# Performance work log

Measured on AMD Instinct MI355X. Metric: run time of the kernel, lower is better.

Reference implementation:

```python
import jax, jax.numpy as jnp
import numpy as np

N = 10000      # nodes
E = 320000     # edges (avg degree 32)
D_IN = 128
D_H = 256
D_C = 32       # comm_dim
D_OUT = 64


def setup_inputs() -> dict:
    key = jax.random.key(0)
    ks = jax.random.split(key, 14)
    p = lambda k, shape: jax.random.normal(k, shape, jnp.float32) * 0.02
    return {
        "x": jax.random.normal(ks[0], (N, D_IN), jnp.float32),
        "edge_index": jax.random.randint(ks[1], (2, E), 0, N),
        "W_in": p(ks[2], (D_IN, D_H)), "b_in": jnp.zeros((D_H,), jnp.float32),
        "Wq": p(ks[3], (D_H, D_C)),   "bq": jnp.zeros((D_C,), jnp.float32),
        "Wk": p(ks[4], (D_H, D_C)),   "bk": jnp.zeros((D_C,), jnp.float32),
        "Wv": p(ks[5], (D_H, D_H)),   "bv": jnp.zeros((D_H,), jnp.float32),
        "W1": p(ks[6], (2 * D_H, D_H)), "b1": jnp.zeros((D_H,), jnp.float32),
        "W2": p(ks[7], (D_H, D_OUT)),  "b2": jnp.zeros((D_OUT,), jnp.float32),
    }


def reference(x, edge_index, W_in, b_in, Wq, bq, Wk, bk, Wv, bv, W1, b1, W2, b2):
    n = x.shape[0]
    h = x @ W_in + b_in                       # [N, D_H]
    q = h @ Wq + bq                           # [N, D_C]
    k = h @ Wk + bk                           # [N, D_C]
    v = h @ Wv + bv                           # [N, D_H]
    scores = (q @ k.T) / np.sqrt(q.shape[-1]).astype(np.float32)  # [N, N]
    # torch: zeros -> scatter 1 at edges -> masked_fill(==0, -inf);
    # edge positions keep value 1.0 ADDED to scores (faithful quirk).
    mask = jnp.full((n, n), -jnp.inf, jnp.float32)
    mask = mask.at[edge_index[0], edge_index[1]].set(1.0)
    w = jax.nn.softmax(scores + mask, axis=-1)
    w = jnp.nan_to_num(w, nan=0.0)            # rows with no edges -> all zeros
    comm = w @ v                              # [N, D_H]
    combined = jnp.concatenate([h, comm], axis=-1)  # [N, 2*D_H]
    return jax.nn.relu(combined @ W1 + b1) @ W2 + b2  # [N, D_OUT]
```

## Files before the change

### kernel.cpp

```cpp
#include <hip/hip_runtime.h>
#include <stdint.h>
#include <stddef.h>

constexpr int N_NODES = 10000;
constexpr int N_EDGES = 320000;
constexpr int DIM_IN  = 128;
constexpr int DIM_H   = 256;
constexpr int DIM_C   = 32;
constexpr int DIM_OUT = 64;
constexpr int DIM_QKV = DIM_C + DIM_C + DIM_H;
constexpr int DIM_QK  = 2 * DIM_C;
constexpr int DIM_CAT = 2 * DIM_H;
constexpr float SCALE = 0.17677669529663687f;
constexpr int MAXD = 192;
constexpr float VSCALE = 64.0f;

#if __has_builtin(__builtin_amdgcn_cvt_pk_f32_fp8) && __has_builtin(__builtin_amdgcn_cvt_pk_fp8_f32)
#define V_FP8 1
#else
#define V_FP8 0
#endif

constexpr size_t alignw(size_t w) { return (w + 15) & ~size_t(15); }
constexpr size_t OFF_DEG    = 0;
constexpr size_t OFF_COL    = alignw(OFF_DEG + N_NODES);
constexpr size_t OFF_QK     = alignw(OFF_COL + (size_t)N_NODES * MAXD);
constexpr size_t OFF_BQKV   = alignw(OFF_QK + (size_t)N_NODES * DIM_QK);
constexpr size_t OFF_VBF    = alignw(OFF_BQKV + DIM_QKV);
constexpr size_t OFF_XBF    = alignw(OFF_VBF + (size_t)N_NODES * DIM_H / 2);
constexpr size_t OFF_CATBF  = alignw(OFF_XBF + (size_t)N_NODES * DIM_IN / 2);
constexpr size_t OFF_WINT   = alignw(OFF_CATBF + (size_t)N_NODES * DIM_CAT / 2);
constexpr size_t OFF_WQKVT  = alignw(OFF_WINT + (size_t)DIM_H * DIM_IN / 2);
constexpr size_t OFF_W1T    = alignw(OFF_WQKVT + (size_t)DIM_QKV * DIM_H / 2);
constexpr size_t OFF_W2T    = alignw(OFF_W1T + (size_t)DIM_H * DIM_CAT / 2);

typedef __attribute__((ext_vector_type(8))) short short8;
typedef __attribute__((ext_vector_type(4))) float floatx4;
typedef __attribute__((ext_vector_type(2))) float floatx2;

__device__ inline unsigned short f2bf(float f) {
    uint32_t u = __builtin_bit_cast(uint32_t, f);
    uint32_t r = (u + 0x7fffu + ((u >> 16) & 1u)) >> 16;
    return (unsigned short)r;
}
__device__ inline float bf2f_lo(uint32_t u) { return __builtin_bit_cast(float, u << 16); }
__device__ inline float bf2f_hi(uint32_t u) { return __builtin_bit_cast(float, u & 0xffff0000u); }

template <bool RELU, int MODE>
__global__ __launch_bounds__(256)
void mfma_gemm(const unsigned short* __restrict__ A, int lda,
               const unsigned short* __restrict__ Bt,
               const float* __restrict__ bias,
               float* __restrict__ Cf, unsigned short* __restrict__ Cb, int ldc,
               int M, int K)
{
    constexpr int BM = 128, BN = 64, PAD = 40;
    __shared__ short As[BM * PAD];
    __shared__ short Bs[BN * PAD];
    const int tid   = threadIdx.x;
    const int wave  = tid >> 6;
    const int lane  = tid & 63;
    const int quad  = lane >> 4;
    const int col16 = lane & 15;
    const int row0  = blockIdx.y * BM;
    const int col0  = blockIdx.x * BN;

    floatx4 acc[2][4] = {};

    const int sr = tid >> 2;
    const int sc = (tid & 3) * 8;

    for (int k0 = 0; k0 < K; k0 += 32) {
        #pragma unroll
        for (int i = 0; i < 2; ++i) {
            int r = sr + i * 64;
            int gr = row0 + r;
            short8 v = {};
            if (gr < M) v = *(const short8*)(A + (size_t)gr * lda + k0 + sc);
            *(short8*)(As + r * PAD + sc) = v;
        }
        {
            short8 v = *(const short8*)(Bt + (size_t)(col0 + sr) * K + k0 + sc);
            *(short8*)(Bs + sr * PAD + sc) = v;
        }
        __syncthreads();
        short8 a0 = *(const short8*)(As + (wave * 32 + col16) * PAD + quad * 8);
        short8 a1 = *(const short8*)(As + (wave * 32 + 16 + col16) * PAD + quad * 8);
        #pragma unroll
        for (int nf = 0; nf < 4; ++nf) {
            short8 b = *(const short8*)(Bs + (nf * 16 + col16) * PAD + quad * 8);
            acc[0][nf] = __builtin_amdgcn_mfma_f32_16x16x32_bf16(a0, b, acc[0][nf], 0, 0, 0);
            acc[1][nf] = __builtin_amdgcn_mfma_f32_16x16x32_bf16(a1, b, acc[1][nf], 0, 0, 0);
        }
        __syncthreads();
    }
    #pragma unroll
    for (int mf = 0; mf < 2; ++mf)
        #pragma unroll
        for (int r = 0; r < 4; ++r) {
            int gr = row0 + wave * 32 + mf * 16 + quad * 4 + r;
            if (gr >= M) continue;
            #pragma unroll
            for (int nf = 0; nf < 4; ++nf) {
                int gc = col0 + nf * 16 + col16;
                float v = acc[mf][nf][r] + bias[gc];
                if (RELU) v = fmaxf(v, 0.f);
                if (MODE == 2) {
                    if (gc < DIM_QK) {
                        Cf[(size_t)gr * DIM_QK + gc] = v;
                    } else {
#if V_FP8
                        int pk = __builtin_amdgcn_cvt_pk_fp8_f32(v * VSCALE, 0.f, 0, false);
                        ((unsigned char*)Cb)[(size_t)gr * DIM_H + (gc - DIM_QK)] =
                            (unsigned char)(pk & 0xff);
#else
                        Cb[(size_t)gr * DIM_H + (gc - DIM_QK)] = f2bf(v);
#endif
                    }
                } else {
                    Cb[(size_t)gr * ldc + gc] = f2bf(v);
                }
            }
        }
}

__global__ __launch_bounds__(256)
void gemm_w1w2(const unsigned short* __restrict__ cat, const unsigned short* __restrict__ W1T,
               const float* __restrict__ b1, const unsigned short* __restrict__ W2T,
               const float* __restrict__ b2, float* __restrict__ out, int M)
{
    constexpr int PAD = 40, TP = 260;
    __shared__ short As[64 * PAD];
    __shared__ short BsTs[64 * TP];
    short* Bs = BsTs;
    short* Ts = BsTs;
    const int tid   = threadIdx.x;
    const int wave  = tid >> 6;
    const int lane  = tid & 63;
    const int quad  = lane >> 4;
    const int col16 = lane & 15;
    const int row0  = blockIdx.x * 64;

    const int sr = tid >> 2;
    const int sc = (tid & 3) * 8;

    floatx4 acc[16] = {};
    for (int k0 = 0; k0 < DIM_CAT; k0 += 32) {
        {
            int gr = row0 + sr;
            short8 v = {};
            if (gr < M) v = *(const short8*)(cat + (size_t)gr * DIM_CAT + k0 + sc);
            *(short8*)(As + sr * PAD + sc) = v;
        }
        #pragma unroll
        for (int p = 0; p < 4; ++p) {
            int r = sr + p * 64;
            *(short8*)(Bs + r * PAD + sc) = *(const short8*)(W1T + (size_t)r * DIM_CAT + k0 + sc);
        }
        __syncthreads();
        short8 a = *(const short8*)(As + (wave * 16 + col16) * PAD + quad * 8);
        #pragma unroll
        for (int nf = 0; nf < 16; ++nf) {
            short8 b = *(const short8*)(Bs + (nf * 16 + col16) * PAD + quad * 8);
            acc[nf] = __builtin_amdgcn_mfma_f32_16x16x32_bf16(a, b, acc[nf], 0, 0, 0);
        }
        __syncthreads();
    }

    #pragma unroll
    for (int nf = 0; nf < 16; ++nf) {
        int gc = nf * 16 + col16;
        float bia = b1[gc];
        #pragma unroll
        for (int r = 0; r < 4; ++r) {
            int lr = wave * 16 + quad * 4 + r;
            float v = fmaxf(acc[nf][r] + bia, 0.f);
            Ts[lr * TP + gc] = (short)f2bf(v);
        }
    }
    __syncthreads();

    floatx4 acc2[4] = {};
    for (int k0 = 0; k0 < DIM_H; k0 += 32) {
        short8 a = *(const short8*)(Ts + (wave * 16 + col16) * TP + k0 + quad * 8);
        #pragma unroll
        for (int nf = 0; nf < 4; ++nf) {
            int brow = nf * 16 + col16;
            short8 b = *(const short8*)(W2T + (size_t)brow * DIM_H + k0 + quad * 8);
            acc2[nf] = __builtin_amdgcn_mfma_f32_16x16x32_bf16(a, b, acc2[nf], 0, 0, 0);
        }
    }
    #pragma unroll
    for (int nf = 0; nf < 4; ++nf) {
        int gc = nf * 16 + col16;
        float bia = b2[gc];
        #pragma unroll
        for (int r = 0; r < 4; ++r) {
            int gr = row0 + wave * 16 + quad * 4 + r;
            if (gr < M) out[(size_t)gr * DIM_OUT + gc] = acc2[nf][r] + bia;
        }
    }
}

__global__ void zero_deg(int* __restrict__ deg) {
    int i = blockIdx.x * blockDim.x + threadIdx.x;
    if (i < N_NODES) deg[i] = 0;
}

__global__ void prep_all(const float* __restrict__ x, const int* __restrict__ ei,
                         const float* __restrict__ W_in,
                         const float* __restrict__ Wq, const float* __restrict__ Wk,
                         const float* __restrict__ Wv,
                         const float* __restrict__ bq, const float* __restrict__ bk,
                         const float* __restrict__ bv,
                         const float* __restrict__ W1, const float* __restrict__ W2,
                         int* __restrict__ deg, int* __restrict__ col,
                         unsigned short* __restrict__ xb,
                         unsigned short* __restrict__ WinT, unsigned short* __restrict__ WqkvT,
                         unsigned short* __restrict__ W1T, unsigned short* __restrict__ W2T,
                         float* __restrict__ bqkv)
{
    int i = blockIdx.x * blockDim.x + threadIdx.x;
    int stride = gridDim.x * blockDim.x;
    for (int e = i; e < N_EDGES; e += stride) {
        int src = ei[e];
        int dst = ei[N_EDGES + e];
        int slot = atomicAdd(&deg[src], 1);
        if (slot < MAXD) col[src * MAXD + slot] = dst;
    }
    for (int idx = i; idx < (N_NODES * DIM_IN) / 8; idx += stride) {
        float4 a = ((const float4*)x)[2 * idx];
        float4 b = ((const float4*)x)[2 * idx + 1];
        uint4 o;
        o.x = (uint32_t)f2bf(a.x) | ((uint32_t)f2bf(a.y) << 16);
        o.y = (uint32_t)f2bf(a.z) | ((uint32_t)f2bf(a.w) << 16);
        o.z = (uint32_t)f2bf(b.x) | ((uint32_t)f2bf(b.y) << 16);
        o.w = (uint32_t)f2bf(b.z) | ((uint32_t)f2bf(b.w) << 16);
        ((uint4*)xb)[idx] = o;
    }
    for (int idx = i; idx < DIM_H * DIM_IN; idx += stride) {
        int n = idx / DIM_IN, k = idx % DIM_IN;
        WinT[idx] = f2bf(W_in[k * DIM_H + n]);
    }
    for (int idx = i; idx < DIM_QKV * DIM_H; idx += stride) {
        int n = idx / DIM_H, k = idx % DIM_H;
        float v = (n < DIM_C)     ? Wq[k * DIM_C + n]
                : (n < 2 * DIM_C) ? Wk[k * DIM_C + (n - DIM_C)]
                                  : Wv[k * DIM_H + (n - 2 * DIM_C)];
        WqkvT[idx] = f2bf(v);
    }
    for (int idx = i; idx < DIM_H * DIM_CAT; idx += stride) {
        int n = idx / DIM_CAT, k = idx % DIM_CAT;
        W1T[idx] = f2bf(W1[k * DIM_H + n]);
    }
    for (int idx = i; idx < DIM_OUT * DIM_H; idx += stride) {
        int n = idx / DIM_H, k = idx % DIM_H;
        W2T[idx] = f2bf(W2[k * DIM_OUT + n]);
    }
    for (int idx = i; idx < DIM_QKV; idx += stride)
        bqkv[idx] = (idx < DIM_C) ? bq[idx]
                  : (idx < 2 * DIM_C) ? bk[idx - DIM_C] : bv[idx - 2 * DIM_C];
}

__global__ __launch_bounds__(256)
void attn_row(const float* __restrict__ qk, const unsigned short* __restrict__ v_tab,
              const int* __restrict__ deg, const int* __restrict__ col,
              unsigned short* __restrict__ cat_bf) {
    __shared__ int   dstS[4][MAXD];
    __shared__ float wS[4][MAXD];
    __shared__ float qS[4][DIM_C];
    const int wave = threadIdx.x >> 6;
    const int lane = threadIdx.x & 63;
    const int row = blockIdx.x * 4 + wave;
    int d = deg[row];
    if (d > MAXD) d = MAXD;
    const int* crow = col + (size_t)row * MAXD;

    for (int p = lane; p < d; p += 64) dstS[wave][p] = crow[p];
    if (lane < DIM_C) qS[wave][lane] = qk[(size_t)row * DIM_QK + lane];
    __syncthreads();

    float mysum = 0.f;
    if (d <= 64) {
        int mydst = (lane < d) ? dstS[wave][lane] : -1;
        bool dup = false;
        #pragma unroll
        for (int k = 0; k < 63; ++k) {
            int other = __shfl(mydst, k, 64);
            dup = dup || (k < lane && other == mydst);
        }
        float w = 0.f;
        if (lane < d && !dup) {
            const float4* kp = (const float4*)(qk + (size_t)mydst * DIM_QK + DIM_C);
            float s = 0.f;
            #pragma unroll
            for (int i = 0; i < DIM_C / 4; ++i) {
                float4 b = kp[i];
                s += qS[wave][4 * i + 0] * b.x + qS[wave][4 * i + 1] * b.y
                   + qS[wave][4 * i + 2] * b.z + qS[wave][4 * i + 3] * b.w;
            }
            w = expf(s * SCALE);
        }
        wS[wave][lane] = w;
        mysum = w;
    } else {
        for (int p = lane; p < d; p += 64) {
            int mydst = dstS[wave][p];
            bool dup = false;
            for (int j = 0; j < p; ++j) dup = dup || (dstS[wave][j] == mydst);
            float w = 0.f;
            if (!dup) {
                const float4* kp = (const float4*)(qk + (size_t)mydst * DIM_QK + DIM_C);
                float s = 0.f;
                #pragma unroll
                for (int i = 0; i < DIM_C / 4; ++i) {
                    float4 b = kp[i];
                    s += qS[wave][4 * i + 0] * b.x + qS[wave][4 * i + 1] * b.y
                       + qS[wave][4 * i + 2] * b.z + qS[wave][4 * i + 3] * b.w;
                }
                w = expf(s * SCALE);
            }
            wS[wave][p] = w;
            mysum += w;
        }
    }
    #pragma unroll
    for (int off = 32; off; off >>= 1) mysum += __shfl_down(mysum, off, 64);
    float total = __shfl(mysum, 0, 64);
#if V_FP8
    float inv = (d > 0 && total > 0.f) ? 1.0f / (total * VSCALE) : 0.f;
#else
    float inv = (d > 0 && total > 0.f) ? 1.0f / total : 0.f;
#endif
    __syncthreads();

    float4 acc = make_float4(0.f, 0.f, 0.f, 0.f);
#if V_FP8
    const uint32_t* vb = (const uint32_t*)v_tab;
#else
    const uint2* vb = (const uint2*)v_tab;
#endif
    for (int p0 = 0; p0 < d; p0 += 16) {
        int j[16]; float w[16];
        #pragma unroll
        for (int t = 0; t < 16; ++t) {
            int idx = p0 + t;
            bool in = idx < d;
            j[t] = in ? dstS[wave][idx] : 0;
            w[t] = in ? wS[wave][idx] : 0.f;
        }
#if V_FP8
        uint32_t r[16];
        #pragma unroll
        for (int t = 0; t < 16; ++t) r[t] = vb[(size_t)j[t] * 64 + lane];
        #pragma unroll
        for (int t = 0; t < 16; ++t) {
            floatx2 lo = __builtin_amdgcn_cvt_pk_f32_fp8(r[t], false);
            floatx2 hi = __builtin_amdgcn_cvt_pk_f32_fp8(r[t], true);
            acc.x += w[t] * lo.x; acc.y += w[t] * lo.y;
            acc.z += w[t] * hi.x; acc.w += w[t] * hi.y;
        }
#else
        uint2 r[16];
        #pragma unroll
        for (int t = 0; t < 16; ++t) r[t] = vb[(size_t)j[t] * 64 + lane];
        #pragma unroll
        for (int t = 0; t < 16; ++t) {
            acc.x += w[t] * bf2f_lo(r[t].x);
            acc.y += w[t] * bf2f_hi(r[t].x);
            acc.z += w[t] * bf2f_lo(r[t].y);
            acc.w += w[t] * bf2f_hi(r[t].y);
        }
#endif
    }
    acc.x *= inv; acc.y *= inv; acc.z *= inv; acc.w *= inv;
    uint2 o;
    o.x = (uint32_t)f2bf(acc.x) | ((uint32_t)f2bf(acc.y) << 16);
    o.y = (uint32_t)f2bf(acc.z) | ((uint32_t)f2bf(acc.w) << 16);
    *(uint2*)(cat_bf + (size_t)row * DIM_CAT + DIM_H + lane * 4) = o;
}

extern "C" void kernel_launch(void* const* d_in, const int* in_sizes, int n_in,
                              void* d_out, int out_size, void* d_ws, size_t ws_size,
                              hipStream_t stream) {
    (void)in_sizes; (void)n_in; (void)out_size; (void)ws_size;
    const float* x    = (const float*)d_in[0];
    const int*   ei   = (const int*)d_in[1];
    const float* W_in = (const float*)d_in[2];
    const float* b_in = (const float*)d_in[3];
    const float* Wq   = (const float*)d_in[4];
    const float* bq   = (const float*)d_in[5];
    const float* Wk   = (const float*)d_in[6];
    const float* bk   = (const float*)d_in[7];
    const float* Wv   = (const float*)d_in[8];
    const float* bv   = (const float*)d_in[9];
    const float* W1   = (const float*)d_in[10];
    const float* b1   = (const float*)d_in[11];
    const float* W2   = (const float*)d_in[12];
    const float* b2   = (const float*)d_in[13];
    float* out = (float*)d_out;

    uint32_t* ws      = (uint32_t*)d_ws;
    int*      deg     = (int*)(ws + OFF_DEG);
    int*      col     = (int*)(ws + OFF_COL);
    float*    qk      = (float*)(ws + OFF_QK);
    float*    bqkv    = (float*)(ws + OFF_BQKV);
    unsigned short* v_tab  = (unsigned short*)(ws + OFF_VBF);
    unsigned short* x_bf   = (unsigned short*)(ws + OFF_XBF);
    unsigned short* cat_bf = (unsigned short*)(ws + OFF_CATBF);
    unsigned short* WinT   = (unsigned short*)(ws + OFF_WINT);
    unsigned short* WqkvT  = (unsigned short*)(ws + OFF_WQKVT);
    unsigned short* W1T    = (unsigned short*)(ws + OFF_W1T);
    unsigned short* W2T    = (unsigned short*)(ws + OFF_W2T);

    zero_deg<<<(N_NODES + 255) / 256, 256, 0, stream>>>(deg);
    prep_all<<<640, 256, 0, stream>>>(x, ei, W_in, Wq, Wk, Wv, bq, bk, bv, W1, W2,
                                      deg, col, x_bf, WinT, WqkvT, W1T, W2T, bqkv);

    const int MB = (N_NODES + 127) / 128;
    mfma_gemm<false, 1><<<dim3(DIM_H / 64, MB), 256, 0, stream>>>(
        x_bf, DIM_IN, WinT, b_in, nullptr, cat_bf, DIM_CAT, N_NODES, DIM_IN);
    mfma_gemm<false, 2><<<dim3(DIM_QKV / 64, MB), 256, 0, stream>>>(
        cat_bf, DIM_CAT, WqkvT, bqkv, qk, v_tab, 0, N_NODES, DIM_H);
    attn_row<<<N_NODES / 4, 256, 0, stream>>>(qk, v_tab, deg, col, cat_bf);
    gemm_w1w2<<<(N_NODES + 63) / 64, 256, 0, stream>>>(
        cat_bf, W1T, b1, W2T, b2, out, N_NODES);
}
```

Baseline: 177.9 us.

## Fuse input projection and QKV GEMMs, convert x to bf16 on the fly

Merges the x@W_in GEMM and the QKV GEMM into one kernel that keeps the h tile in shared memory, so h is not reloaded from global memory for the second GEMM. The fp32 to bf16 conversion of x moves into that GEMM's load path, which drops the separate x_bf buffer and its pass in the prep kernel. The weight-transpose loops in prep now read coalesced and write strided. The zero_deg kernel becomes a memset, and the duplicate-check loop in attention is bounded by degree. The fused kernel uses a large shared-memory footprint and one block per 64 rows, which may reduce occupancy.

```diff
diff --git a/kernel.cpp b/kernel.cpp
--- a/kernel.cpp
+++ b/kernel.cpp
@@ -14,6 +14,8 @@
 constexpr float SCALE = 0.17677669529663687f;
 constexpr int MAXD = 192;
 constexpr float VSCALE = 64.0f;
+constexpr int PAD = 40;
+constexpr int HP  = 264;
 
 #if __has_builtin(__builtin_amdgcn_cvt_pk_f32_fp8) && __has_builtin(__builtin_amdgcn_cvt_pk_fp8_f32)
 #define V_FP8 1
@@ -22,21 +24,22 @@
 #endif
 
 constexpr size_t alignw(size_t w) { return (w + 15) & ~size_t(15); }
-constexpr size_t OFF_DEG    = 0;
-constexpr size_t OFF_COL    = alignw(OFF_DEG + N_NODES);
-constexpr size_t OFF_QK     = alignw(OFF_COL + (size_t)N_NODES * MAXD);
-constexpr size_t OFF_BQKV   = alignw(OFF_QK + (size_t)N_NODES * DIM_QK);
-constexpr size_t OFF_VBF    = alignw(OFF_BQKV + DIM_QKV);
-constexpr size_t OFF_XBF    = alignw(OFF_VBF + (size_t)N_NODES * DIM_H / 2);
-constexpr size_t OFF_CATBF  = alignw(OFF_XBF + (size_t)N_NODES * DIM_IN / 2);
-constexpr size_t OFF_WINT   = alignw(OFF_CATBF + (size_t)N_NODES * DIM_CAT / 2);
-constexpr size_t OFF_WQKVT  = alignw(OFF_WINT + (size_t)DIM_H * DIM_IN / 2);
-constexpr size_t OFF_W1T    = alignw(OFF_WQKVT + (size_t)DIM_QKV * DIM_H / 2);
-constexpr size_t OFF_W2T    = alignw(OFF_W1T + (size_t)DIM_H * DIM_CAT / 2);
+constexpr size_t OFF_DEG   = 0;
+constexpr size_t OFF_COL   = alignw(OFF_DEG + N_NODES);
+constexpr size_t OFF_QK    = alignw(OFF_COL + (size_t)N_NODES * MAXD);
+constexpr size_t OFF_BQKV  = alignw(OFF_QK + (size_t)N_NODES * DIM_QK);
+constexpr size_t OFF_VT    = alignw(OFF_BQKV + DIM_QKV);
+constexpr size_t OFF_CATBF = alignw(OFF_VT + (size_t)N_NODES * DIM_H / 2);
+constexpr size_t OFF_WINT  = alignw(OFF_CATBF + (size_t)N_NODES * DIM_CAT / 2);
+constexpr size_t OFF_WQKVT = alignw(OFF_WINT + (size_t)DIM_H * DIM_IN / 2);
+constexpr size_t OFF_W1T   = alignw(OFF_WQKVT + (size_t)DIM_QKV * DIM_H / 2);
+constexpr size_t OFF_W2T   = alignw(OFF_W1T + (size_t)DIM_H * DIM_CAT / 2);
 
 typedef __attribute__((ext_vector_type(8))) short short8;
 typedef __attribute__((ext_vector_type(4))) float floatx4;
 typedef __attribute__((ext_vector_type(2))) float floatx2;
+
+#define MFMA16 __builtin_amdgcn_mfma_f32_16x16x32_bf16
 
 __device__ inline unsigned short f2bf(float f) {
     uint32_t u = __builtin_bit_cast(uint32_t, f);
@@ -46,220 +49,156 @@
 __device__ inline float bf2f_lo(uint32_t u) { return __builtin_bit_cast(float, u << 16); }
 __device__ inline float bf2f_hi(uint32_t u) { return __builtin_bit_cast(float, u & 0xffff0000u); }
 
-template <bool RELU, int MODE>
+__global__ void prep(const int* __restrict__ ei,
+                     const float* __restrict__ W_in,
+                     const float* __restrict__ Wq, const float* __restrict__ Wk,
+                     const float* __restrict__ Wv,
+                     const float* __restrict__ bq, const float* __restrict__ bk,
+                     const float* __restrict__ bv,
+                     const float* __restrict__ W1, const float* __restrict__ W2,
+                     int* __restrict__ deg, int* __restrict__ col,
+                     unsigned short* __restrict__ WinT, unsigned short* __restrict__ WqkvT,
+                     unsigned short* __restrict__ W1T, unsigned short* __restrict__ W2T,
+                     float* __restrict__ bqkv)
+{
+    const int i0 = blockIdx.x * blockDim.x + threadIdx.x;
+    const int stride = gridDim.x * blockDim.x;
+    for (int e = i0; e < N_EDGES; e += stride) {
+        int src = ei[e];
+        int dst = ei[N_EDGES + e];
+        int slot = atomicAdd(&deg[src], 1);
+        if (slot < MAXD) col[src * MAXD + slot] = dst;
+    }
+    for (int idx = i0; idx < DIM_IN * DIM_H; idx += stride) {
+        int k = idx >> 8, n = idx & 255;
+        WinT[n * DIM_IN + k] = f2bf(W_in[idx]);
+    }
+    for (int idx = i0; idx < DIM_H * DIM_C; idx += stride) {
+        int k = idx >> 5, n = idx & 31;
+        WqkvT[n * DIM_H + k] = f2bf(Wq[idx]);
+    }
+    for (int idx = i0; idx < DIM_H * DIM_C; idx += stride) {
+        int k = idx >> 5, n = idx & 31;
+        WqkvT[(DIM_C + n) * DIM_H + k] = f2bf(Wk[idx]);
+    }
+    for (int idx = i0; idx < DIM_H * DIM_H; idx += stride) {
+        int k = idx >> 8, n = idx & 255;
+        WqkvT[(2 * DIM_C + n) * DIM_H + k] = f2bf(Wv[idx]);
+    }
+    for (int idx = i0; idx < DIM_CAT * DIM_H; idx += stride) {
+        int k = idx >> 8, n = idx & 255;
+        W1T[n * DIM_CAT + k] = f2bf(W1[idx]);
+    }
+    for (int idx = i0; idx < DIM_H * DIM_OUT; idx += stride) {
+        int k = idx >> 6, n = idx & 63;
+        W2T[n * DIM_H + k] = f2bf(W2[idx]);
+    }
+    for (int idx = i0; idx < DIM_QKV; idx += stride)
+        bqkv[idx] = (idx < DIM_C) ? bq[idx]
+                  : (idx < 2 * DIM_C) ? bk[idx - DIM_C] : bv[idx - 2 * DIM_C];
+}
+
 __global__ __launch_bounds__(256)
-void mfma_gemm(const unsigned short* __restrict__ A, int lda,
-               const unsigned short* __restrict__ Bt,
-               const float* __restrict__ bias,
-               float* __restrict__ Cf, unsigned short* __restrict__ Cb, int ldc,
-               int M, int K)
+void gemm12(const float* __restrict__ x,
+            const unsigned short* __restrict__ WinT, const float* __restrict__ b_in,
+            const unsigned short* __restrict__ WqkvT, const float* __restrict__ bqkv,
+            unsigned short* __restrict__ cat_bf, float* __restrict__ qk,
+            unsigned short* __restrict__ v_tab)
 {
-    constexpr int BM = 128, BN = 64, PAD = 40;
-    __shared__ short As[BM * PAD];
-    __shared__ short Bs[BN * PAD];
+    __shared__ short hS[64 * HP];
+    __shared__ short Bs[320 * PAD];
+    short* As = Bs + 256 * PAD;
     const int tid   = threadIdx.x;
     const int wave  = tid >> 6;
     const int lane  = tid & 63;
     const int quad  = lane >> 4;
     const int col16 = lane & 15;
-    const int row0  = blockIdx.y * BM;
-    const int col0  = blockIdx.x * BN;
-
-    floatx4 acc[2][4] = {};
-
-    const int sr = tid >> 2;
-    const int sc = (tid & 3) * 8;
-
-    for (int k0 = 0; k0 < K; k0 += 32) {
-        #pragma unroll
-        for (int i = 0; i < 2; ++i) {
-            int r = sr + i * 64;
-            int gr = row0 + r;
-            short8 v = {};
-            if (gr < M) v = *(const short8*)(A + (size_t)gr * lda + k0 + sc);
-            *(short8*)(As + r * PAD + sc) = v;
-        }
-        {
-            short8 v = *(const short8*)(Bt + (size_t)(col0 + sr) * K + k0 + sc);
-            *(short8*)(Bs + sr * PAD + sc) = v;
-        }
-        __syncthreads();
-        short8 a0 = *(const short8*)(As + (wave * 32 + col16) * PAD + quad * 8);
-        short8 a1 = *(const short8*)(As + (wave * 32 + 16 + col16) * PAD + quad * 8);
-        #pragma unroll
-        for (int nf = 0; nf < 4; ++nf) {
-            short8 b = *(const short8*)(Bs + (nf * 16 + col16) * PAD + quad * 8);
-            acc[0][nf] = __builtin_amdgcn_mfma_f32_16x16x32_bf16(a0, b, acc[0][nf], 0, 0, 0);
-            acc[1][nf] = __builtin_amdgcn_mfma_f32_16x16x32_bf16(a1, b, acc[1][nf], 0, 0, 0);
-        }
-        __syncthreads();
-    }
-    #pragma unroll
-    for (int mf = 0; mf < 2; ++mf)
-        #pragma unroll
-        for (int r = 0; r < 4; ++r) {
-            int gr = row0 + wave * 32 + mf * 16 + quad * 4 + r;
-            if (gr >= M) continue;
-            #pragma unroll
-            for (int nf = 0; nf < 4; ++nf) {
-                int gc = col0 + nf * 16 + col16;
-                float v = acc[mf][nf][r] + bias[gc];
-                if (RELU) v = fmaxf(v, 0.f);
-                if (MODE == 2) {
-                    if (gc < DIM_QK) {
-                        Cf[(size_t)gr * DIM_QK + gc] = v;
-                    } else {
-#if V_FP8
-                        int pk = __builtin_amdgcn_cvt_pk_fp8_f32(v * VSCALE, 0.f, 0, false);
-                        ((unsigned char*)Cb)[(size_t)gr * DIM_H + (gc - DIM_QK)] =
-                            (unsigned char)(pk & 0xff);
-#else
-                        Cb[(size_t)gr * DIM_H + (gc - DIM_QK)] = f2bf(v);
-#endif
-                    }
-                } else {
-                    Cb[(size_t)gr * ldc + gc] = f2bf(v);
-                }
-            }
-        }
-}
-
-__global__ __launch_bounds__(256)
-void gemm_w1w2(const unsigned short* __restrict__ cat, const unsigned short* __restrict__ W1T,
-               const float* __restrict__ b1, const unsigned short* __restrict__ W2T,
-               const float* __restrict__ b2, float* __restrict__ out, int M)
-{
-    constexpr int PAD = 40, TP = 260;
-    __shared__ short As[64 * PAD];
-    __shared__ short BsTs[64 * TP];
-    short* Bs = BsTs;
-    short* Ts = BsTs;
-    const int tid   = threadIdx.x;
-    const int wave  = tid >> 6;
-    const int lane  = tid & 63;
-    const int quad  = lane >> 4;
-    const int col16 = lane & 15;
+    const int sr    = tid >> 2;
+    const int sc    = (tid & 3) * 8;
     const int row0  = blockIdx.x * 64;
 
-    const int sr = tid >> 2;
-    const int sc = (tid & 3) * 8;
-
     floatx4 acc[16] = {};
-    for (int k0 = 0; k0 < DIM_CAT; k0 += 32) {
+    for (int k0 = 0; k0 < DIM_IN; k0 += 32) {
         {
             int gr = row0 + sr;
-            short8 v = {};
-            if (gr < M) v = *(const short8*)(cat + (size_t)gr * DIM_CAT + k0 + sc);
-            *(short8*)(As + sr * PAD + sc) = v;
+            float4 a = {}, b = {};
+            if (gr < N_NODES) {
+                const float4* xp = (const float4*)(x + (size_t)gr * DIM_IN + k0 + sc);
+                a = xp[0]; b = xp[1];
+            }
+            uint4 o;
+            o.x = (uint32_t)f2bf(a.x) | ((uint32_t)f2bf(a.y) << 16);
+            o.y = (uint32_t)f2bf(a.z) | ((uint32_t)f2bf(a.w) << 16);
+            o.z = (uint32_t)f2bf(b.x) | ((uint32_t)f2bf(b.y) << 16);
+            o.w = (uint32_t)f2bf(b.z) | ((uint32_t)f2bf(b.w) << 16);
+            *(uint4*)(As + sr * PAD + sc) = o;
         }
         #pragma unroll
         for (int p = 0; p < 4; ++p) {
             int r = sr + p * 64;
-            *(short8*)(Bs + r * PAD + sc) = *(const short8*)(W1T + (size_t)r * DIM_CAT + k0 + sc);
-        }
-        __syncthreads();
-        short8 a = *(const short8*)(As + (wave * 16 + col16) * PAD + quad * 8);
+            *(short8*)(Bs + r * PAD + sc) = *(const short8*)(WinT + (size_t)r * DIM_IN + k0 + sc);
+        }
+        __syncthreads();
+        short8 af = *(const short8*)(As + (wave * 16 + col16) * PAD + quad * 8);
         #pragma unroll
         for (int nf = 0; nf < 16; ++nf) {
-            short8 b = *(const short8*)(Bs + (nf * 16 + col16) * PAD + quad * 8);
-            acc[nf] = __builtin_amdgcn_mfma_f32_16x16x32_bf16(a, b, acc[nf], 0, 0, 0);
-        }
-        __syncthreads();
-    }
-
+            short8 bf = *(const short8*)(Bs + (nf * 16 + col16) * PAD + quad * 8);
+            acc[nf] = MFMA16(af, bf, acc[nf], 0, 0, 0);
+        }
+        __syncthreads();
+    }
     #pragma unroll
     for (int nf = 0; nf < 16; ++nf) {
         int gc = nf * 16 + col16;
-        float bia = b1[gc];
+        float bia = b_in[gc];
         #pragma unroll
         for (int r = 0; r < 4; ++r) {
             int lr = wave * 16 + quad * 4 + r;
-            float v = fmaxf(acc[nf][r] + bia, 0.f);
-            Ts[lr * TP + gc] = (short)f2bf(v);
+            unsigned short hv = f2bf(acc[nf][r] + bia);
+            hS[lr * HP + gc] = (short)hv;
+            if (row0 + lr < N_NODES) cat_bf[(size_t)(row0 + lr) * DIM_CAT + gc] = hv;
         }
     }
     __syncthreads();
 
-    floatx4 acc2[4] = {};
+    floatx4 acc2[20] = {};
     for (int k0 = 0; k0 < DIM_H; k0 += 32) {
-        short8 a = *(const short8*)(Ts + (wave * 16 + col16) * TP + k0 + quad * 8);
-        #pragma unroll
-        for (int nf = 0; nf < 4; ++nf) {
-            int brow = nf * 16 + col16;
-            short8 b = *(const short8*)(W2T + (size_t)brow * DIM_H + k0 + quad * 8);
-            acc2[nf] = __builtin_amdgcn_mfma_f32_16x16x32_bf16(a, b, acc2[nf], 0, 0, 0);
-        }
+        #pragma unroll
+        for (int p = 0; p < 5; ++p) {
+            int r = sr + p * 64;
+            *(short8*)(Bs + r * PAD + sc) = *(const short8*)(WqkvT + (size_t)r * DIM_H + k0 + sc);
+        }
+        __syncthreads();
+        short8 af = *(const short8*)(hS + (wave * 16 + col16) * HP + k0 + quad * 8);
+        #pragma unroll
+        for (int nf = 0; nf < 20; ++nf) {
+            short8 bf = *(const short8*)(Bs + (nf * 16 + col16) * PAD + quad * 8);
+            acc2[nf] = MFMA16(af, bf, acc2[nf], 0, 0, 0);
+        }
+        __syncthreads();
     }
     #pragma unroll
-    for (int nf = 0; nf < 4; ++nf) {
+    for (int nf = 0; nf < 20; ++nf) {
         int gc = nf * 16 + col16;
-        float bia = b2[gc];
+        float bia = bqkv[gc];
         #pragma unroll
         for (int r = 0; r < 4; ++r) {
             int gr = row0 + wave * 16 + quad * 4 + r;
-            if (gr < M) out[(size_t)gr * DIM_OUT + gc] = acc2[nf][r] + bia;
-        }
-    }
-}
-
-__global__ void zero_deg(int* __restrict__ deg) {
-    int i = blockIdx.x * blockDim.x + threadIdx.x;
-    if (i < N_NODES) deg[i] = 0;
-}
-
-__global__ void prep_all(const float* __restrict__ x, const int* __restrict__ ei,
-                         const float* __restrict__ W_in,
-                         const float* __restrict__ Wq, const float* __restrict__ Wk,
-                         const float* __restrict__ Wv,
-                         const float* __restrict__ bq, const float* __restrict__ bk,
-                         const float* __restrict__ bv,
-                         const float* __restrict__ W1, const float* __restrict__ W2,
-                         int* __restrict__ deg, int* __restrict__ col,
-                         unsigned short* __restrict__ xb,
-                         unsigned short* __restrict__ WinT, unsigned short* __restrict__ WqkvT,
-                         unsigned short* __restrict__ W1T, unsigned short* __restrict__ W2T,
-                         float* __restrict__ bqkv)
-{
-    int i = blockIdx.x * blockDim.x + threadIdx.x;
-    int stride = gridDim.x * blockDim.x;
-    for (int e = i; e < N_EDGES; e += stride) {
-        int src = ei[e];
-        int dst = ei[N_EDGES + e];
-        int slot = atomicAdd(&deg[src], 1);
-        if (slot < MAXD) col[src * MAXD + slot] = dst;
-    }
-    for (int idx = i; idx < (N_NODES * DIM_IN) / 8; idx += stride) {
-        float4 a = ((const float4*)x)[2 * idx];
-        float4 b = ((const float4*)x)[2 * idx + 1];
-        uint4 o;
-        o.x = (uint32_t)f2bf(a.x) | ((uint32_t)f2bf(a.y) << 16);
-        o.y = (uint32_t)f2bf(a.z) | ((uint32_t)f2bf(a.w) << 16);
-        o.z = (uint32_t)f2bf(b.x) | ((uint32_t)f2bf(b.y) << 16);
-        o.w = (uint32_t)f2bf(b.z) | ((uint32_t)f2bf(b.w) << 16);
-        ((uint4*)xb)[idx] = o;
-    }
-    for (int idx = i; idx < DIM_H * DIM_IN; idx += stride) {
-        int n = idx / DIM_IN, k = idx % DIM_IN;
-        WinT[idx] = f2bf(W_in[k * DIM_H + n]);
-    }
-    for (int idx = i; idx < DIM_QKV * DIM_H; idx += stride) {
-        int n = idx / DIM_H, k = idx % DIM_H;
-        float v = (n < DIM_C)     ? Wq[k * DIM_C + n]
-                : (n < 2 * DIM_C) ? Wk[k * DIM_C + (n - DIM_C)]
-                                  : Wv[k * DIM_H + (n - 2 * DIM_C)];
-        WqkvT[idx] = f2bf(v);
-    }
-    for (int idx = i; idx < DIM_H * DIM_CAT; idx += stride) {
-        int n = idx / DIM_CAT, k = idx % DIM_CAT;
-        W1T[idx] = f2bf(W1[k * DIM_H + n]);
-    }
-    for (int idx = i; idx < DIM_OUT * DIM_H; idx += stride) {
-        int n = idx / DIM_H, k = idx % DIM_H;
-        W2T[idx] = f2bf(W2[k * DIM_OUT + n]);
-    }
-    for (int idx = i; idx < DIM_QKV; idx += stride)
-        bqkv[idx] = (idx < DIM_C) ? bq[idx]
-                  : (idx < 2 * DIM_C) ? bk[idx - DIM_C] : bv[idx - 2 * DIM_C];
+            if (gr >= N_NODES) continue;
+            float v = acc2[nf][r] + bia;
+            if (gc < DIM_QK) {
+                qk[(size_t)gr * DIM_QK + gc] = v;
+            } else {
+#if V_FP8
+                int pk = __builtin_amdgcn_cvt_pk_fp8_f32(v * VSCALE, 0.f, 0, false);
+                ((unsigned char*)v_tab)[(size_t)gr * DIM_H + (gc - DIM_QK)] =
+                    (unsigned char)(pk & 0xff);
+#else
+                v_tab[(size_t)gr * DIM_H + (gc - DIM_QK)] = f2bf(v);
+#endif
+            }
+        }
+    }
 }
 
 __global__ __launch_bounds__(256)
@@ -284,10 +223,9 @@
     if (d <= 64) {
         int mydst = (lane < d) ? dstS[wave][lane] : -1;
         bool dup = false;
-        #pragma unroll
-        for (int k = 0; k < 63; ++k) {
-            int other = __shfl(mydst, k, 64);
-            dup = dup || (k < lane && other == mydst);
+        for (int k2 = 0; k2 < d - 1; ++k2) {
+            int other = __shfl(mydst, k2, 64);
+            dup = dup || (k2 < lane && other == mydst);
         }
         float w = 0.f;
         if (lane < d && !dup) {
@@ -380,6 +318,84 @@
     *(uint2*)(cat_bf + (size_t)row * DIM_CAT + DIM_H + lane * 4) = o;
 }
 
+__global__ __launch_bounds__(256)
+void gemm_w1w2(const unsigned short* __restrict__ cat, const unsigned short* __restrict__ W1T,
+               const float* __restrict__ b1, const unsigned short* __restrict__ W2T,
+               const float* __restrict__ b2, float* __restrict__ out, int M)
+{
+    constexpr int TP = 260;
+    __shared__ short As[64 * PAD];
+    __shared__ short BsTs[64 * TP];
+    short* Bs = BsTs;
+    short* Ts = BsTs;
+    const int tid   = threadIdx.x;
+    const int wave  = tid >> 6;
+    const int lane  = tid & 63;
+    const int quad  = lane >> 4;
+    const int col16 = lane & 15;
+    const int row0  = blockIdx.x * 64;
+
+    const int sr = tid >> 2;
+    const int sc = (tid & 3) * 8;
+
+    floatx4 acc[16] = {};
+    for (int k0 = 0; k0 < DIM_CAT; k0 += 32) {
+        {
+            int gr = row0 + sr;
+            short8 v = {};
+            if (gr < M) v = *(const short8*)(cat + (size_t)gr * DIM_CAT + k0 + sc);
+            *(short8*)(As + sr * PAD + sc) = v;
+        }
+        #pragma unroll
+        for (int p = 0; p < 4; ++p) {
+            int r = sr + p * 64;
+            *(short8*)(Bs + r * PAD + sc) = *(const short8*)(W1T + (size_t)r * DIM_CAT + k0 + sc);
+        }
+        __syncthreads();
+        short8 a = *(const short8*)(As + (wave * 16 + col16) * PAD + quad * 8);
+        #pragma unroll
+        for (int nf = 0; nf < 16; ++nf) {
+            short8 b = *(const short8*)(Bs + (nf * 16 + col16) * PAD + quad * 8);
+            acc[nf] = MFMA16(a, b, acc[nf], 0, 0, 0);
+        }
+        __syncthreads();
+    }
+
+    #pragma unroll
+    for (int nf = 0; nf < 16; ++nf) {
+        int gc = nf * 16 + col16;
+        float bia = b1[gc];
+        #pragma unroll
+        for (int r = 0; r < 4; ++r) {
+            int lr = wave * 16 + quad * 4 + r;
+            float v = fmaxf(acc[nf][r] + bia, 0.f);
+            Ts[lr * TP + gc] = (short)f2bf(v);
+        }
+    }
+    __syncthreads();
+
+    floatx4 acc2[4] = {};
+    for (int k0 = 0; k0 < DIM_H; k0 += 32) {
+        short8 a = *(const short8*)(Ts + (wave * 16 + col16) * TP + k0 + quad * 8);
+        #pragma unroll
+        for (int nf = 0; nf < 4; ++nf) {
+            int brow = nf * 16 + col16;
+            short8 b = *(const short8*)(W2T + (size_t)brow * DIM_H + k0 + quad * 8);
+            acc2[nf] = MFMA16(a, b, acc2[nf], 0, 0, 0);
+        }
+    }
+    #pragma unroll
+    for (int nf = 0; nf < 4; ++nf) {
+        int gc = nf * 16 + col16;
+        float bia = b2[gc];
+        #pragma unroll
+        for (int r = 0; r < 4; ++r) {
+            int gr = row0 + wave * 16 + quad * 4 + r;
+            if (gr < M) out[(size_t)gr * DIM_OUT + gc] = acc2[nf][r] + bia;
+        }
+    }
+}
+
 extern "C" void kernel_launch(void* const* d_in, const int* in_sizes, int n_in,
                               void* d_out, int out_size, void* d_ws, size_t ws_size,
                               hipStream_t stream) {
@@ -405,23 +421,18 @@
     int*      col     = (int*)(ws + OFF_COL);
     float*    qk      = (float*)(ws + OFF_QK);
     float*    bqkv    = (float*)(ws + OFF_BQKV);
-    unsigned short* v_tab  = (unsigned short*)(ws + OFF_VBF);
-    unsigned short* x_bf   = (unsigned short*)(ws + OFF_XBF);
+    unsigned short* v_tab  = (unsigned short*)(ws + OFF_VT);
     unsigned short* cat_bf = (unsigned short*)(ws + OFF_CATBF);
     unsigned short* WinT   = (unsigned short*)(ws + OFF_WINT);
     unsigned short* WqkvT  = (unsigned short*)(ws + OFF_WQKVT);
     unsigned short* W1T    = (unsigned short*)(ws + OFF_W1T);
     unsigned short* W2T    = (unsigned short*)(ws + OFF_W2T);
 
-    zero_deg<<<(N_NODES + 255) / 256, 256, 0, stream>>>(deg);
-    prep_all<<<640, 256, 0, stream>>>(x, ei, W_in, Wq, Wk, Wv, bq, bk, bv, W1, W2,
-                                      deg, col, x_bf, WinT, WqkvT, W1T, W2T, bqkv);
-
-    const int MB = (N_NODES + 127) / 128;
-    mfma_gemm<false, 1><<<dim3(DIM_H / 64, MB), 256, 0, stream>>>(
-        x_bf, DIM_IN, WinT, b_in, nullptr, cat_bf, DIM_CAT, N_NODES, DIM_IN);
-    mfma_gemm<false, 2><<<dim3(DIM_QKV / 64, MB), 256, 0, stream>>>(
-        cat_bf, DIM_CAT, WqkvT, bqkv, qk, v_tab, 0, N_NODES, DIM_H);
+    hipMemsetAsync(deg, 0, N_NODES * sizeof(int), stream);
+    prep<<<640, 256, 0, stream>>>(ei, W_in, Wq, Wk, Wv, bq, bk, bv, W1, W2,
+                                  deg, col, WinT, WqkvT, W1T, W2T, bqkv);
+    gemm12<<<(N_NODES + 63) / 64, 256, 0, stream>>>(
+        x, WinT, b_in, WqkvT, bqkv, cat_bf, qk, v_tab);
     attn_row<<<N_NODES / 4, 256, 0, stream>>>(qk, v_tab, deg, col, cat_bf);
     gemm_w1w2<<<(N_NODES + 63) / 64, 256, 0, stream>>>(
         cat_bf, W1T, b1, W2T, b2, out, N_NODES);
```

Result: slower. 189.3 us (+6.4%).
